# Kernel optimization log

Hardware: AMD Instinct MI355X
Metric: run time of the kernel (lower is better)

Reference implementation:

```python
import jax, jax.numpy as jnp
import numpy as np


def setup_inputs() -> dict:
    key = jax.random.key(0)
    k1, k2 = jax.random.split(key)
    B, C, LIN = 8, 128, 65536
    K, LOUT = 9, 16384
    x = jax.random.normal(k1, (B, C, LIN), dtype=jnp.float32)
    neighbours = jax.random.randint(k2, (K, LOUT), 0, LIN, dtype=jnp.int64)
    return {"x": x, "neighbours": neighbours}


def reference(x, neighbours):
    # x: (B, C, locs_in); neighbours: (k, locs_out)
    # gather -> (B, C, k, locs_out), max over k axis -> (B, C, locs_out)
    gathered = x[:, :, neighbours]
    return jnp.max(gathered, axis=-2)
```

## Files before the change

kernel.cpp:

```cpp
#include <hip/hip_runtime.h>
#include <hip/hip_fp16.h>


#define B_DIM 8
#define C_DIM 128
#define LIN 65536
#define K_DIM 9
#define LOUT 16384
#define BC (B_DIM * C_DIM)
#define NTHREADS 1024

__global__ __launch_bounds__(NTHREADS) void fused_rowmax(
    const float4* __restrict__ x4,
    const int* __restrict__ nbr,
    float* __restrict__ out)
{
    __shared__ __half sh[LIN];
    const int tid = threadIdx.x;
    const int bc  = blockIdx.x;

    const float4* __restrict__ xr = x4 + (size_t)bc * (LIN / 4);
#pragma unroll
    for (int r = 0; r < LIN / 4 / NTHREADS; ++r) {
        const int g = r * NTHREADS + tid;
        const float4 v = xr[g];
        ushort4 w;
        w.x = __half_as_ushort(__float2half_rn(v.x));
        w.y = __half_as_ushort(__float2half_rn(v.y));
        w.z = __half_as_ushort(__float2half_rn(v.z));
        w.w = __half_as_ushort(__float2half_rn(v.w));
        *(ushort4*)(sh + 4 * g) = w;
    }
    __syncthreads();

    float* __restrict__ orow = out + (size_t)bc * LOUT;
#pragma unroll 1
    for (int it = 0; it < LOUT / (4 * NTHREADS); ++it) {
        const int l0 = it * (4 * NTHREADS) + 4 * tid;
        float4 res = make_float4(-INFINITY, -INFINITY, -INFINITY, -INFINITY);
#pragma unroll
        for (int k = 0; k < K_DIM; ++k) {
            const int4 id = *(const int4*)(nbr + k * LOUT + l0);
            res.x = fmaxf(res.x, __half2float(sh[id.x]));
            res.y = fmaxf(res.y, __half2float(sh[id.y]));
            res.z = fmaxf(res.z, __half2float(sh[id.z]));
            res.w = fmaxf(res.w, __half2float(sh[id.w]));
        }
        *(float4*)(orow + l0) = res;
    }
}

extern "C" void kernel_launch(void* const* d_in, const int* in_sizes, int n_in,
                              void* d_out, int out_size, void* d_ws, size_t ws_size,
                              hipStream_t stream) {
    const float4* x   = (const float4*)d_in[0];
    const int*    nbr = (const int*)d_in[1];
    float*        out = (float*)d_out;
    (void)d_ws; (void)ws_size; (void)in_sizes; (void)n_in; (void)out_size;

    fused_rowmax<<<dim3(BC), dim3(NTHREADS), 0, stream>>>(x, nbr, out);
}
```

Before: 394.2 us.

## Process multiple rows per block and prefetch next row during gather

Each block now handles four rows sequentially, loading the next row's x data into registers while the current row's gather-max runs from LDS, then writing the converted halves to LDS after a barrier. This aims to hide the global-load phase behind the LDS gather, which previously serialized since only one block fit per CU. It adds register pressure (staged fp16 data and float4 buffers per thread) and extra barriers, and reduces the grid to 256 blocks.

```diff
diff --git a/kernel.cpp b/kernel.cpp
--- a/kernel.cpp
+++ b/kernel.cpp
@@ -2,51 +2,93 @@
 #include <hip/hip_fp16.h>
 
 
-#define B_DIM 8
-#define C_DIM 128
 #define LIN 65536
 #define K_DIM 9
 #define LOUT 16384
-#define BC (B_DIM * C_DIM)
-#define NTHREADS 1024
+#define BC 1024
+#define NT 1024
+#define RPB 4
+#define NCHUNK (LIN / 4 / NT)
 
-__global__ __launch_bounds__(NTHREADS) void fused_rowmax(
+__global__ __launch_bounds__(NT) void fused_rowmax_pipe(
     const float4* __restrict__ x4,
     const int* __restrict__ nbr,
     float* __restrict__ out)
 {
     __shared__ __half sh[LIN];
     const int tid = threadIdx.x;
-    const int bc  = blockIdx.x;
+    const int row0 = blockIdx.x * RPB;
 
-    const float4* __restrict__ xr = x4 + (size_t)bc * (LIN / 4);
+    {
+        const float4* __restrict__ xr = x4 + (size_t)row0 * (LIN / 4);
 #pragma unroll
-    for (int r = 0; r < LIN / 4 / NTHREADS; ++r) {
-        const int g = r * NTHREADS + tid;
-        const float4 v = xr[g];
-        ushort4 w;
-        w.x = __half_as_ushort(__float2half_rn(v.x));
-        w.y = __half_as_ushort(__float2half_rn(v.y));
-        w.z = __half_as_ushort(__float2half_rn(v.z));
-        w.w = __half_as_ushort(__float2half_rn(v.w));
-        *(ushort4*)(sh + 4 * g) = w;
+        for (int i = 0; i < NCHUNK; ++i) {
+            const int g = i * NT + tid;
+            const float4 v = xr[g];
+            ushort4 w;
+            w.x = __half_as_ushort(__float2half_rn(v.x));
+            w.y = __half_as_ushort(__float2half_rn(v.y));
+            w.z = __half_as_ushort(__float2half_rn(v.z));
+            w.w = __half_as_ushort(__float2half_rn(v.w));
+            *(ushort4*)(sh + 4 * g) = w;
+        }
     }
     __syncthreads();
 
-    float* __restrict__ orow = out + (size_t)bc * LOUT;
 #pragma unroll 1
-    for (int it = 0; it < LOUT / (4 * NTHREADS); ++it) {
-        const int l0 = it * (4 * NTHREADS) + 4 * tid;
-        float4 res = make_float4(-INFINITY, -INFINITY, -INFINITY, -INFINITY);
+    for (int r = 0; r < RPB; ++r) {
+        const bool pf = (r + 1 < RPB);
+        const float4* __restrict__ xn = x4 + (size_t)(row0 + r + 1) * (LIN / 4);
+        float* __restrict__ orow = out + (size_t)(row0 + r) * LOUT;
+
+        ushort4 pk[NCHUNK];
+        float4  buf[4];
+
+        if (pf) {
 #pragma unroll
-        for (int k = 0; k < K_DIM; ++k) {
-            const int4 id = *(const int4*)(nbr + k * LOUT + l0);
-            res.x = fmaxf(res.x, __half2float(sh[id.x]));
-            res.y = fmaxf(res.y, __half2float(sh[id.y]));
-            res.z = fmaxf(res.z, __half2float(sh[id.z]));
-            res.w = fmaxf(res.w, __half2float(sh[id.w]));
+            for (int i = 0; i < 4; ++i) buf[i] = xn[i * NT + tid];
         }
-        *(float4*)(orow + l0) = res;
+
+#pragma unroll
+        for (int it = 0; it < 4; ++it) {
+            const int l0 = it * (4 * NT) + 4 * tid;
+            float4 res = make_float4(-INFINITY, -INFINITY, -INFINITY, -INFINITY);
+#pragma unroll
+            for (int k = 0; k < K_DIM; ++k) {
+                const int4 id = *(const int4*)(nbr + k * LOUT + l0);
+                res.x = fmaxf(res.x, __half2float(sh[id.x]));
+                res.y = fmaxf(res.y, __half2float(sh[id.y]));
+                res.z = fmaxf(res.z, __half2float(sh[id.z]));
+                res.w = fmaxf(res.w, __half2float(sh[id.w]));
+            }
+            *(float4*)(orow + l0) = res;
+
+            if (pf) {
+#pragma unroll
+                for (int i = 0; i < 4; ++i) {
+                    const float4 v = buf[i];
+                    ushort4 w;
+                    w.x = __half_as_ushort(__float2half_rn(v.x));
+                    w.y = __half_as_ushort(__float2half_rn(v.y));
+                    w.z = __half_as_ushort(__float2half_rn(v.z));
+                    w.w = __half_as_ushort(__float2half_rn(v.w));
+                    pk[4 * it + i] = w;
+                }
+                if (it < 3) {
+#pragma unroll
+                    for (int i = 0; i < 4; ++i)
+                        buf[i] = xn[(4 * (it + 1) + i) * NT + tid];
+                }
+            }
+        }
+
+        __syncthreads();
+        if (pf) {
+#pragma unroll
+            for (int c = 0; c < NCHUNK; ++c)
+                *(ushort4*)(sh + 4 * (c * NT + tid)) = pk[c];
+        }
+        __syncthreads();
     }
 }
 
@@ -58,5 +100,5 @@
     float*        out = (float*)d_out;
     (void)d_ws; (void)ws_size; (void)in_sizes; (void)n_in; (void)out_size;
 
-    fused_rowmax<<<dim3(BC), dim3(NTHREADS), 0, stream>>>(x, nbr, out);
+    fused_rowmax_pipe<<<dim3(BC / RPB), dim3(NT), 0, stream>>>(x, nbr, out);
 }
```

Result: slower. 479.2 us (+21.6%).
